# Kernel tuning notes

Hardware: AMD Instinct MI355X
Metric: run time of the kernel (lower is better)

Reference implementation:

```python
import jax, jax.numpy as jnp
import numpy as np
from jax import lax

HEADS = 8
LN_EPS = 1e-5


def setup_inputs() -> dict:
    key = jax.random.key(0)
    k = jax.random.split(key, 8)
    B, C, H, W, r = 4, 64, 64, 64, 4
    T = H * W
    x = jax.random.normal(k[0], (B, C, H, W), dtype=jnp.float32)
    conv_w = jax.random.normal(k[1], (C, C, r, r), dtype=jnp.float32) * 0.02  # OIHW
    conv_b = jnp.zeros((C,), dtype=jnp.float32)
    ln_g = jnp.ones((C,), dtype=jnp.float32)
    ln_b = jnp.zeros((C,), dtype=jnp.float32)
    Wqkv = jax.random.normal(k[2], (C, 3 * C), dtype=jnp.float32) * 0.02  # to_qvk (no bias)
    W0 = jax.random.normal(k[3], (C, C), dtype=jnp.float32) * 0.02  # output proj (no bias)
    E = jax.random.normal(k[4], (T, T // 4), dtype=jnp.float32)  # Linformer proj (randn in torch fwd)
    return {"x": x, "conv_w": conv_w, "conv_b": conv_b, "ln_g": ln_g,
            "ln_b": ln_b, "Wqkv": Wqkv, "W0": W0, "E": E}


def _layernorm2d(y, g, b):
    # LayerNorm over channel dim of NCHW (torch: permute to NHWC, LN last dim)
    yt = y.transpose(0, 2, 3, 1)  # b h w c
    mu = yt.mean(-1, keepdims=True)
    var = ((yt - mu) ** 2).mean(-1, keepdims=True)
    yt = (yt - mu) * lax.rsqrt(var + LN_EPS) * g + b
    return yt.transpose(0, 3, 1, 2)


def reference(x, conv_w, conv_b, ln_g, ln_b, Wqkv, W0, E):
    B, C, H, W = x.shape
    T = H * W
    dh = C // HEADS
    r = conv_w.shape[-1]

    # reducer: conv(stride=r) + LayerNorm2d. NOTE: faithful to the torch module,
    # this result is computed but NEVER used by the output (dead code in source).
    red = lax.conv_general_dilated(x, conv_w, (r, r), 'VALID',
                                   dimension_numbers=('NCHW', 'OIHW', 'NCHW'))
    red = red + conv_b[None, :, None, None]
    _red = _layernorm2d(red, ln_g, ln_b)  # unused, matches source

    # tokens from full-resolution x: b c h w -> b (h w) c
    xf = x.reshape(B, C, T).transpose(0, 2, 1)  # [B,T,C]
    qkv = xf @ Wqkv  # [B,T,3C]
    # rearrange 'b t (d k h)' with k=3, h=HEADS -> composite order (d, k, h)
    qkv = qkv.reshape(B, T, dh, 3, HEADS)
    q = qkv[:, :, :, 0, :].transpose(0, 3, 1, 2)  # [B,h,T,d]
    kk = qkv[:, :, :, 1, :].transpose(0, 3, 1, 2)
    v = qkv[:, :, :, 2, :].transpose(0, 3, 1, 2)

    # Linformer low-rank projection of V and K: [B,h,T,d] x [T,k] -> [B,h,k,d]
    v = jnp.einsum('bhjd,jk->bhkd', v, E)
    kk = jnp.einsum('bhjd,jk->bhkd', kk, E)

    scale = dh ** -0.5
    scores = jnp.einsum('bhid,bhjd->bhij', q, kk) * scale  # [B,h,T,k]
    attn = jax.nn.softmax(scores, axis=-1)
    out = jnp.einsum('bhij,bhjd->bhid', attn, v)  # [B,h,T,d]

    out = out.transpose(0, 2, 1, 3).reshape(B, T, C)  # b h i d -> b i (h d)
    out = out @ W0  # [B,T,C]
    return out.transpose(0, 2, 1).reshape(B, C, H, W)
```

## Files before the change

### kernel.cpp

```cpp
#include <hip/hip_runtime.h>

#define T_DIM 4096
#define KD    1024
#define SCALE 0.35355339059327373f

typedef __attribute__((ext_vector_type(8))) short bf16x8;
typedef __attribute__((ext_vector_type(4))) short bf16x4;
typedef __attribute__((ext_vector_type(4))) float f32x4;

__device__ inline unsigned short f2bf(float f) {
  unsigned u = __float_as_uint(f);
  unsigned r = u + 0x7fffu + ((u >> 16) & 1u);
  return (unsigned short)(r >> 16);
}

__device__ inline unsigned cvt_pk_bf16(float a, float b) {
  unsigned ua = __float_as_uint(a); ua += 0x7fffu + ((ua >> 16) & 1u);
  unsigned ub = __float_as_uint(b); ub += 0x7fffu + ((ub >> 16) & 1u);
  return (ua >> 16) | (ub & 0xffff0000u);
}

__device__ inline unsigned pk_trunc(float a, float b) {
  return (__float_as_uint(a) >> 16) | (__float_as_uint(b) & 0xffff0000u);
}

__device__ inline bf16x4 mk4(unsigned lo, unsigned hi) {
  union { unsigned u[2]; bf16x4 v; } x; x.u[0] = lo; x.u[1] = hi; return x.v;
}

__device__ inline bf16x8 mk8(unsigned a, unsigned b, unsigned c, unsigned d) {
  union { unsigned u[4]; bf16x8 v; } x;
  x.u[0] = a; x.u[1] = b; x.u[2] = c; x.u[3] = d; return x.v;
}

__device__ inline f32x4 mfma16(bf16x4 a, bf16x4 b, f32x4 c) {
  bf16x8 a8 = {}, b8 = {};
  a8[0] = a[0]; a8[1] = a[1]; a8[2] = a[2]; a8[3] = a[3];
  b8[0] = b[0]; b8[1] = b[1]; b8[2] = b[2]; b8[3] = b[3];
  return __builtin_amdgcn_mfma_f32_16x16x32_bf16(a8, b8, c, 0, 0, 0);
}

__global__ __launch_bounds__(256) void k_front(const float* __restrict__ x,
                                               const float* __restrict__ E,
                                               const float* __restrict__ Wqkv,
                                               float* __restrict__ partial,
                                               float* __restrict__ Q) {
  const int bid = blockIdx.x;
  const int tid = threadIdx.x;

  if (bid < 512) {
    const int kb = bid & 7;
    const int b  = (bid >> 3) & 3;
    const int s  = bid >> 5;
    const int k0 = kb * 128;
    const int lane = tid & 63;
    const int w = tid >> 6;
    const int li = lane & 15, lg = lane >> 4;

    f32x4 acc[4][2] = {};
#pragma unroll 2
    for (int tb = 0; tb < 8; ++tb) {
      const int tbase = s * 256 + tb * 32 + lg * 8;
      bf16x8 bq[2];
#pragma unroll
      for (int nt = 0; nt < 2; ++nt) {
        const int kcol = k0 + w * 32 + nt * 16 + li;
        float bv[8];
#pragma unroll
        for (int j = 0; j < 8; ++j)
          bv[j] = E[(size_t)(tbase + j) * KD + kcol];
        bq[nt] = mk8(cvt_pk_bf16(bv[0], bv[1]), cvt_pk_bf16(bv[2], bv[3]),
                     cvt_pk_bf16(bv[4], bv[5]), cvt_pk_bf16(bv[6], bv[7]));
      }
#pragma unroll
      for (int mt = 0; mt < 4; ++mt) {
        const float* ap = x + ((size_t)b * 64 + mt * 16 + li) * T_DIM + tbase;
        float4 a0 = *(const float4*)(ap);
        float4 a1 = *(const float4*)(ap + 4);
        bf16x8 af8 = mk8(cvt_pk_bf16(a0.x, a0.y), cvt_pk_bf16(a0.z, a0.w),
                         cvt_pk_bf16(a1.x, a1.y), cvt_pk_bf16(a1.z, a1.w));
        acc[mt][0] = __builtin_amdgcn_mfma_f32_16x16x32_bf16(af8, bq[0], acc[mt][0], 0, 0, 0);
        acc[mt][1] = __builtin_amdgcn_mfma_f32_16x16x32_bf16(af8, bq[1], acc[mt][1], 0, 0, 0);
      }
    }
    float* pb = partial + ((size_t)s * 4 + b) * (64 * KD);
#pragma unroll
    for (int mt = 0; mt < 4; ++mt)
#pragma unroll
      for (int nt = 0; nt < 2; ++nt) {
        const int row = mt * 16 + lg * 4;
        const int col = k0 + w * 32 + nt * 16 + li;
#pragma unroll
        for (int reg = 0; reg < 4; ++reg)
          pb[(size_t)(row + reg) * KD + col] = acc[mt][nt][reg];
      }
  } else {
    const int idx = bid - 512;
    const int g  = idx & 7;
    const int tt = (idx >> 3) & 15;
    const int b  = idx >> 7;
    const int t  = tt * 256 + tid;
    const int col0 = g * 24;

    float acc[8];
#pragma unroll
    for (int j = 0; j < 8; ++j) acc[j] = 0.f;
    const float* xb = x + (size_t)b * 64 * T_DIM + t;
#pragma unroll 4
    for (int c = 0; c < 64; ++c) {
      float xv = xb[(size_t)c * T_DIM];
      const float* wr = Wqkv + c * 192 + col0;
#pragma unroll
      for (int h = 0; h < 8; ++h) acc[h] += xv * wr[h];
    }
#pragma unroll
    for (int h = 0; h < 8; ++h)
      Q[(((size_t)(b * 8 + h)) * 8 + g) * T_DIM + t] = acc[h];
  }
}

__global__ __launch_bounds__(256) void k_xkv(const float* __restrict__ partial,
                                             const float* __restrict__ Wqkv,
                                             uint2* __restrict__ Kg,
                                             unsigned short* __restrict__ Vg) {
  __shared__ unsigned short XPs[64 * 72];
  const int kb = blockIdx.x;
  const int h  = blockIdx.y;
  const int b  = blockIdx.z;
  const int tid = threadIdx.x;

  {
    const int kk = tid & 63;
    const int cg = tid >> 6;
#pragma unroll
    for (int u = 0; u < 16; ++u) {
      const int c = cg * 16 + u;
      const size_t src = (size_t)c * KD + kb * 64 + kk;
      float a = 0.f;
#pragma unroll
      for (int s = 0; s < 16; ++s)
        a += partial[((size_t)s * 4 + b) * (64 * KD) + src];
      XPs[c * 72 + kk] = f2bf(a);
    }
  }
  __syncthreads();

  const int klocal = tid & 63;
  const int sel    = (tid >> 6) & 1;
  const int dg     = tid >> 7;
  const int k      = kb * 64 + klocal;

  float acc[4];
#pragma unroll
  for (int d = 0; d < 4; ++d) acc[d] = 0.f;
#pragma unroll 4
  for (int c = 0; c < 64; ++c) {
    float xv = __uint_as_float((unsigned)XPs[c * 72 + klocal] << 16);
    const float* wr = Wqkv + c * 192 + (sel + 1) * 8 + h;
#pragma unroll
    for (int d = 0; d < 4; ++d) acc[d] += xv * wr[(dg * 4 + d) * 24];
  }

  const int bh = b * 8 + h;
  if (sel == 0) {
    uint2* kg = Kg + (size_t)bh * 2048;
    kg[dg * 1024 + k] = make_uint2(cvt_pk_bf16(acc[0] * SCALE, acc[1] * SCALE),
                                   cvt_pk_bf16(acc[2] * SCALE, acc[3] * SCALE));
  } else {
#pragma unroll
    for (int d = 0; d < 4; ++d)
      Vg[(size_t)(bh * 8 + dg * 4 + d) * KD + k] = f2bf(acc[d]);
  }
}

#define VT_PITCH 1032
__global__ __launch_bounds__(256) void k_attn(const float* __restrict__ Q,
                                              const uint2* __restrict__ Kg,
                                              const unsigned short* __restrict__ Vg,
                                              float* __restrict__ O) {
  __shared__ unsigned short Kt[2 * 1024 * 4];
  __shared__ unsigned short Vt[9 * VT_PITCH];
  const int bh = blockIdx.x;
  const int tid = threadIdx.x;

  const uint2* kg = Kg + (size_t)bh * 2048;
  uint2* kt2 = (uint2*)Kt;
#pragma unroll
  for (int it = 0; it < 8; ++it)
    kt2[it * 256 + tid] = kg[it * 256 + tid];
  const unsigned* vg = (const unsigned*)(Vg + (size_t)bh * 8192);
#pragma unroll
  for (int dd = 0; dd < 8; ++dd) {
#pragma unroll
    for (int it = 0; it < 2; ++it) {
      const int j2 = it * 256 + tid;
      *(unsigned*)(Vt + dd * VT_PITCH + j2 * 2) = vg[dd * 512 + j2];
    }
  }
#pragma unroll
  for (int it = 0; it < 2; ++it)
    *(unsigned*)(Vt + 8 * VT_PITCH + (it * 256 + tid) * 2) = 0x3F803F80u;
  __syncthreads();

  const int lane = tid & 63, w = tid >> 6;
  const int li = lane & 15, lg = lane >> 4;
  const int i0w = blockIdx.y * 128 + w * 32;

  bf16x4 qf[2] = {bf16x4{}, bf16x4{}};
  if (lane < 32) {
#pragma unroll
    for (int it2 = 0; it2 < 2; ++it2) {
      const float* qp = Q + ((size_t)bh * 8 + lg * 4) * T_DIM + i0w + it2 * 16 + li;
      qf[it2] = mk4(cvt_pk_bf16(qp[0], qp[T_DIM]),
                    cvt_pk_bf16(qp[2 * T_DIM], qp[3 * T_DIM]));
    }
  }

  f32x4 accO[2] = {f32x4{0.f, 0.f, 0.f, 0.f}, f32x4{0.f, 0.f, 0.f, 0.f}};
#pragma unroll 2
  for (int jt = 0; jt < 1024; jt += 16) {
    bf16x4 kf = {};
    if (lane < 32) kf = *(const bf16x4*)(&Kt[(size_t)(lg * 1024 + jt + li) * 4]);
    bf16x4 vf = {};
    if (li < 9) vf = *(const bf16x4*)(&Vt[li * VT_PITCH + jt + lg * 4]);
#pragma unroll
    for (int it2 = 0; it2 < 2; ++it2) {
      f32x4 st = mfma16(kf, qf[it2], f32x4{0.f, 0.f, 0.f, 0.f});
      f32x4 p;
      p[0] = __expf(st[0]); p[1] = __expf(st[1]);
      p[2] = __expf(st[2]); p[3] = __expf(st[3]);
      bf16x4 pf = mk4(pk_trunc(p[0], p[1]), pk_trunc(p[2], p[3]));
      accO[it2] = mfma16(vf, pf, accO[it2]);
    }
  }

  const int b = bh >> 3, h = bh & 7;
#pragma unroll
  for (int it2 = 0; it2 < 2; ++it2) {
    float l = __shfl(accO[it2][0], 32 + li);
    float inv = 1.0f / l;
    if (lane < 32) {
      const int i = i0w + it2 * 16 + li;
      float4 o = make_float4(accO[it2][0] * inv, accO[it2][1] * inv,
                             accO[it2][2] * inv, accO[it2][3] * inv);
      *(float4*)(O + ((size_t)b * T_DIM + i) * 64 + h * 8 + lg * 4) = o;
    }
  }
}

__global__ __launch_bounds__(256) void k_out(const float* __restrict__ O,
                                             const float* __restrict__ W0,
                                             float* __restrict__ out) {
  const int cg_ = blockIdx.x;
  const int tt = blockIdx.y;
  const int b  = blockIdx.z;
  const int t  = tt * 256 + threadIdx.x;
  const int col0 = cg_ * 8;

  float acc[8];
#pragma unroll
  for (int j = 0; j < 8; ++j) acc[j] = 0.f;
  const float* orow = O + ((size_t)b * T_DIM + t) * 64;
#pragma unroll
  for (int c0 = 0; c0 < 64; c0 += 4) {
    float4 v = *(const float4*)(orow + c0);
    float ov[4] = {v.x, v.y, v.z, v.w};
#pragma unroll
    for (int u = 0; u < 4; ++u) {
      const float* wr = W0 + (c0 + u) * 64 + col0;
#pragma unroll
      for (int j = 0; j < 8; ++j) acc[j] += ov[u] * wr[j];
    }
  }
#pragma unroll
  for (int j = 0; j < 8; ++j)
    out[((size_t)b * 64 + col0 + j) * T_DIM + t] = acc[j];
}

extern "C" void kernel_launch(void* const* d_in, const int* in_sizes, int n_in,
                              void* d_out, int out_size, void* d_ws, size_t ws_size,
                              hipStream_t stream) {
  const float* x    = (const float*)d_in[0];
  const float* Wqkv = (const float*)d_in[5];
  const float* W0   = (const float*)d_in[6];
  const float* E    = (const float*)d_in[7];
  float* out = (float*)d_out;

  float* Q           = (float*)d_ws;
  float* O           = Q + 1048576;
  float* partial     = O + 1048576;
  uint2* Kg          = (uint2*)(partial + 4194304);
  unsigned short* Vg = (unsigned short*)(Kg + 65536);

  k_front <<<dim3(1024),     256, 0, stream>>>(x, E, Wqkv, partial, Q);
  k_xkv   <<<dim3(16, 8, 4), 256, 0, stream>>>(partial, Wqkv, Kg, Vg);
  k_attn  <<<dim3(32, 32),   256, 0, stream>>>(Q, Kg, Vg, O);
  k_out   <<<dim3(8, 16, 4), 256, 0, stream>>>(O, W0, out);
}
```

Before: 154.0 us.

## Fuse output projection into attention kernel via per-head atomic accumulation

Removes the separate output-projection kernel and the intermediate O buffer. Each attention block stages its normalized per-head output in shared memory, multiplies it by the head's 8-row slice of W0, and atomically adds partial results into the NCHW output. The front kernel zeroes the output buffer first. This trades the O write/read and one launch for eight fp32 atomic adds per output element and nondeterministic summation order.

```diff
diff --git a/kernel.cpp b/kernel.cpp
--- a/kernel.cpp
+++ b/kernel.cpp
@@ -44,9 +44,12 @@
                                                const float* __restrict__ E,
                                                const float* __restrict__ Wqkv,
                                                float* __restrict__ partial,
-                                               float* __restrict__ Q) {
+                                               float* __restrict__ Q,
+                                               float* __restrict__ out) {
   const int bid = blockIdx.x;
   const int tid = threadIdx.x;
+
+  ((float4*)out)[(size_t)bid * 256 + tid] = make_float4(0.f, 0.f, 0.f, 0.f);
 
   if (bid < 512) {
     const int kb = bid & 7;
@@ -177,11 +180,14 @@
 __global__ __launch_bounds__(256) void k_attn(const float* __restrict__ Q,
                                               const uint2* __restrict__ Kg,
                                               const unsigned short* __restrict__ Vg,
-                                              float* __restrict__ O) {
-  __shared__ unsigned short Kt[2 * 1024 * 4];
+                                              const float* __restrict__ W0,
+                                              float* __restrict__ out) {
+  __shared__ __attribute__((aligned(16))) unsigned short Kt[2 * 1024 * 4];
   __shared__ unsigned short Vt[9 * VT_PITCH];
+  __shared__ float W0s[512];
   const int bh = blockIdx.x;
   const int tid = threadIdx.x;
+  const int b = bh >> 3, h = bh & 7;
 
   const uint2* kg = Kg + (size_t)bh * 2048;
   uint2* kt2 = (uint2*)Kt;
@@ -200,6 +206,8 @@
 #pragma unroll
   for (int it = 0; it < 2; ++it)
     *(unsigned*)(Vt + 8 * VT_PITCH + (it * 256 + tid) * 2) = 0x3F803F80u;
+  W0s[tid]       = W0[h * 512 + tid];
+  W0s[tid + 256] = W0[h * 512 + tid + 256];
   __syncthreads();
 
   const int lane = tid & 63, w = tid >> 6;
@@ -234,47 +242,32 @@
     }
   }
 
-  const int b = bh >> 3, h = bh & 7;
+  __syncthreads();
+  float* OwW = (float*)Kt + w * 256;
+
 #pragma unroll
   for (int it2 = 0; it2 < 2; ++it2) {
     float l = __shfl(accO[it2][0], 32 + li);
     float inv = 1.0f / l;
     if (lane < 32) {
-      const int i = i0w + it2 * 16 + li;
       float4 o = make_float4(accO[it2][0] * inv, accO[it2][1] * inv,
                              accO[it2][2] * inv, accO[it2][3] * inv);
-      *(float4*)(O + ((size_t)b * T_DIM + i) * 64 + h * 8 + lg * 4) = o;
-    }
-  }
-}
-
-__global__ __launch_bounds__(256) void k_out(const float* __restrict__ O,
-                                             const float* __restrict__ W0,
-                                             float* __restrict__ out) {
-  const int cg_ = blockIdx.x;
-  const int tt = blockIdx.y;
-  const int b  = blockIdx.z;
-  const int t  = tt * 256 + threadIdx.x;
-  const int col0 = cg_ * 8;
-
-  float acc[8];
-#pragma unroll
-  for (int j = 0; j < 8; ++j) acc[j] = 0.f;
-  const float* orow = O + ((size_t)b * T_DIM + t) * 64;
-#pragma unroll
-  for (int c0 = 0; c0 < 64; c0 += 4) {
-    float4 v = *(const float4*)(orow + c0);
-    float ov[4] = {v.x, v.y, v.z, v.w};
-#pragma unroll
-    for (int u = 0; u < 4; ++u) {
-      const float* wr = W0 + (c0 + u) * 64 + col0;
-#pragma unroll
-      for (int j = 0; j < 8; ++j) acc[j] += ov[u] * wr[j];
-    }
-  }
-#pragma unroll
-  for (int j = 0; j < 8; ++j)
-    out[((size_t)b * 64 + col0 + j) * T_DIM + t] = acc[j];
+      *(float4*)(OwW + (it2 * 16 + li) * 8 + lg * 4) = o;
+    }
+  }
+
+  const int tok = lane & 31, ch = lane >> 5;
+  float ov[8];
+#pragma unroll
+  for (int d = 0; d < 8; ++d) ov[d] = OwW[tok * 8 + d];
+#pragma unroll 4
+  for (int j = 0; j < 32; ++j) {
+    const int c = ch * 32 + j;
+    float a = 0.f;
+#pragma unroll
+    for (int d = 0; d < 8; ++d) a += ov[d] * W0s[d * 64 + c];
+    atomicAdd(out + ((size_t)b * 64 + c) * T_DIM + i0w + tok, a);
+  }
 }
 
 extern "C" void kernel_launch(void* const* d_in, const int* in_sizes, int n_in,
@@ -287,13 +280,11 @@
   float* out = (float*)d_out;
 
   float* Q           = (float*)d_ws;
-  float* O           = Q + 1048576;
-  float* partial     = O + 1048576;
+  float* partial     = Q + 1048576;
   uint2* Kg          = (uint2*)(partial + 4194304);
   unsigned short* Vg = (unsigned short*)(Kg + 65536);
 
-  k_front <<<dim3(1024),     256, 0, stream>>>(x, E, Wqkv, partial, Q);
+  k_front <<<dim3(1024),     256, 0, stream>>>(x, E, Wqkv, partial, Q, out);
   k_xkv   <<<dim3(16, 8, 4), 256, 0, stream>>>(partial, Wqkv, Kg, Vg);
-  k_attn  <<<dim3(32, 32),   256, 0, stream>>>(Q, Kg, Vg, O);
-  k_out   <<<dim3(8, 16, 4), 256, 0, stream>>>(O, W0, out);
-}
+  k_attn  <<<dim3(32, 32),   256, 0, stream>>>(Q, Kg, Vg, W0, out);
+}
```

Result: faster. 150.5 us (-2.3%).
